# Optimization experiments

Measured on AMD Instinct MI355X. Metric: run time of the kernel, lower is better.

The kernel has to match this reference:

```python
import jax, jax.numpy as jnp
import numpy as np

B, S, D, H = 4, 2048, 1024, 16
HD = D // H


def setup_inputs() -> dict:
    key = jax.random.key(0)
    ks = jax.random.split(key, 5)
    s_in = 1.0 / np.sqrt(D)
    return {
        "x": jax.random.normal(ks[0], (B, S, D), dtype=jnp.float32),
        "W_attn": jax.random.uniform(ks[1], (D, 3 * D), dtype=jnp.float32, minval=-s_in, maxval=s_in),
        "b_attn": jax.random.uniform(ks[2], (3 * D,), dtype=jnp.float32, minval=-s_in, maxval=s_in),
        "W_proj": jax.random.uniform(ks[3], (D, D), dtype=jnp.float32, minval=-s_in, maxval=s_in),
        "b_proj": jax.random.uniform(ks[4], (D,), dtype=jnp.float32, minval=-s_in, maxval=s_in),
    }


def reference(x, W_attn, b_attn, W_proj, b_proj):
    b, s, d = x.shape
    qkv = x @ W_attn + b_attn                      # [B,S,3D]
    q, k, v = jnp.split(qkv, 3, axis=-1)
    # [B,H,S,HD]
    q = q.reshape(b, s, H, HD).transpose(0, 2, 1, 3)
    k = k.reshape(b, s, H, HD).transpose(0, 2, 1, 3)
    v = v.reshape(b, s, H, HD).transpose(0, 2, 1, 3)
    scale = 1.0 / np.sqrt(HD)
    att = jnp.einsum("bhqd,bhkd->bhqk", q, k) * scale
    causal = jnp.tril(jnp.ones((s, s), dtype=bool))
    att = jnp.where(causal[None, None], att, -jnp.inf)
    att = jax.nn.softmax(att, axis=-1)
    y = jnp.einsum("bhqk,bhkd->bhqd", att, v)      # [B,H,S,HD]
    y = y.transpose(0, 2, 1, 3).reshape(b, s, d)
    return y @ W_proj + b_proj
```

## Files before the change

kernel.cpp:

```cpp
#include <hip/hip_runtime.h>

#define B_  4
#define S_  2048
#define D_  1024
#define H_  16
#define HD_ 64
#define BS_ (B_*S_)

typedef _Float16 f16;
typedef _Float16 f16_8 __attribute__((ext_vector_type(8)));
typedef _Float16 f16_4 __attribute__((ext_vector_type(4)));
typedef float    f32_4 __attribute__((ext_vector_type(4)));
typedef unsigned int u32;

#define MFMA32(a,b,c) __builtin_amdgcn_mfma_f32_16x16x32_f16(a, b, c, 0, 0, 0)
#define MFMA16(a,b,c) __builtin_amdgcn_mfma_f32_16x16x16f16(a, b, c, 0, 0, 0)
#define NEG_INF (-__builtin_inff())

__device__ inline void gl_lds16(const f16* g, f16* lds_base, int chunk_base) {
    __builtin_amdgcn_global_load_lds(
        (const __attribute__((address_space(1))) u32*)g,
        (__attribute__((address_space(3))) u32*)(lds_base + (size_t)chunk_base * 8),
        16, 0, 0);
}

__global__ __launch_bounds__(256) void prep(
    const float* __restrict__ X,  f16* __restrict__ Xh,
    const float* __restrict__ Wa, f16* __restrict__ Wta)
{
    __shared__ f16 T[64][72];
    const int t = threadIdx.x;
    const int bid = blockIdx.x;
    if (bid < 4096) {
        const size_t i = ((size_t)bid * 256 + t) * 8;
        float4 a = *(const float4*)&X[i];
        float4 b = *(const float4*)&X[i + 4];
        f16 h[8] = {(f16)a.x,(f16)a.y,(f16)a.z,(f16)a.w,
                    (f16)b.x,(f16)b.y,(f16)b.z,(f16)b.w};
        *(uint4*)&Xh[i] = *(const uint4*)h;
        return;
    }
    const int idx = bid - 4096;
    const int n0 = (idx % 48) * 64, k0 = (idx / 48) * 64;
    const int nl4 = (t & 15) * 4;
    #pragma unroll
    for (int r = 0; r < 4; r++) {
        const int kl = (t >> 4) + r * 16;
        float4 v = *(const float4*)&Wa[(size_t)(k0 + kl) * 3072 + n0 + nl4];
        T[nl4 + 0][kl] = (f16)v.x;
        T[nl4 + 1][kl] = (f16)v.y;
        T[nl4 + 2][kl] = (f16)v.z;
        T[nl4 + 3][kl] = (f16)v.w;
    }
    __syncthreads();
    const int nr = t >> 2, kc = (t & 3) * 16;
    *(uint4*)&Wta[(size_t)(n0 + nr) * 1024 + k0 + kc]     = *(uint4*)&T[nr][kc];
    *(uint4*)&Wta[(size_t)(n0 + nr) * 1024 + k0 + kc + 8] = *(uint4*)&T[nr][kc + 8];
}

__global__ __launch_bounds__(256) void trans_w(
    const float* __restrict__ W, f16* __restrict__ Wt, int ncols)
{
    __shared__ f16 T[64][72];
    const int t = threadIdx.x;
    const int n0 = blockIdx.x * 64, k0 = blockIdx.y * 64;
    const int nl4 = (t & 15) * 4;
    #pragma unroll
    for (int r = 0; r < 4; r++) {
        const int kl = (t >> 4) + r * 16;
        float4 v = *(const float4*)&W[(size_t)(k0 + kl) * ncols + n0 + nl4];
        T[nl4 + 0][kl] = (f16)v.x;
        T[nl4 + 1][kl] = (f16)v.y;
        T[nl4 + 2][kl] = (f16)v.z;
        T[nl4 + 3][kl] = (f16)v.w;
    }
    __syncthreads();
    const int nr = t >> 2, kc = (t & 3) * 16;
    *(uint4*)&Wt[(size_t)(n0 + nr) * 1024 + k0 + kc]     = *(uint4*)&T[nr][kc];
    *(uint4*)&Wt[(size_t)(n0 + nr) * 1024 + k0 + kc + 8] = *(uint4*)&T[nr][kc + 8];
}

__global__ __launch_bounds__(512, 2) void qkv_gemm(
    const f16*   __restrict__ Xh,
    const f16*   __restrict__ Wta,
    const float* __restrict__ bias,
    f16* __restrict__ Qb, f16* __restrict__ Kb, f16* __restrict__ Vt)
{
    __shared__ f16 lds[73728];

    const int t    = threadIdx.x;
    const int lane = t & 63;
    const int w    = t >> 6;
    const int quad = lane >> 4, l15 = lane & 15;
    const int wr = w >> 2, wc = w & 3;
    const int m0 = blockIdx.x * 128;
    const int n0 = blockIdx.y * 256;
    const int wb = t & 448;

    int aoff[2], boff[4];
    #pragma unroll
    for (int c = 0; c < 2; c++) {
        const int i = c*512 + t, row = i >> 3, sl = i & 7;
        aoff[c] = row*1024 + ((sl ^ (row & 7)) << 3);
    }
    #pragma unroll
    for (int c = 0; c < 4; c++) {
        const int i = c*512 + t, row = i >> 3, sl = i & 7;
        boff[c] = row*1024 + ((sl ^ (row & 7)) << 3);
    }
    int fa[4][2], fb[4][2];
    #pragma unroll
    for (int mi = 0; mi < 4; mi++)
        #pragma unroll
        for (int kk = 0; kk < 2; kk++)
            fa[mi][kk] = (wr*64 + mi*16 + l15)*64 + (((kk*4 + quad) ^ (l15 & 7)) << 3);
    #pragma unroll
    for (int ni = 0; ni < 4; ni++)
        #pragma unroll
        for (int kk = 0; kk < 2; kk++)
            fb[ni][kk] = (wc*64 + ni*16 + l15)*64 + (((kk*4 + quad) ^ (l15 & 7)) << 3);

    const f16* Ag = Xh  + (size_t)m0 * 1024;
    const f16* Bg = Wta + (size_t)n0 * 1024;

    f32_4 acc[4][4] = {};

    #pragma unroll
    for (int c = 0; c < 2; c++) gl_lds16(Ag + aoff[c],       lds,                c*512 + wb);
    #pragma unroll
    for (int c = 0; c < 4; c++) gl_lds16(Bg + boff[c],       lds + 8192,         c*512 + wb);
    #pragma unroll
    for (int c = 0; c < 2; c++) gl_lds16(Ag + 64 + aoff[c],  lds + 24576,        c*512 + wb);
    #pragma unroll
    for (int c = 0; c < 4; c++) gl_lds16(Bg + 64 + boff[c],  lds + 24576 + 8192, c*512 + wb);
    asm volatile("s_waitcnt vmcnt(6)" ::: "memory");
    __builtin_amdgcn_s_barrier();
    asm volatile("" ::: "memory");

    int cur = 0;
    #pragma unroll 1
    for (int T = 0; T < 16; T++) {
        f16* buf        = lds + cur*24576;
        const int nxt   = cur ? cur - 1 : 2;
        f16* nbuf       = lds + nxt*24576;
        const bool st   = (T < 14);
        const int  kt2  = (T + 2) * 64;

        if (st) {
            #pragma unroll
            for (int c = 0; c < 2; c++)
                gl_lds16(Ag + kt2 + aoff[c], nbuf, c*512 + wb);
        }
        f16_8 af[4][2], bf[2][2];
        #pragma unroll
        for (int mi = 0; mi < 4; mi++)
            #pragma unroll
            for (int kk = 0; kk < 2; kk++)
                af[mi][kk] = *(const f16_8*)&buf[fa[mi][kk]];
        #pragma unroll
        for (int ni = 0; ni < 2; ni++)
            #pragma unroll
            for (int kk = 0; kk < 2; kk++)
                bf[ni][kk] = *(const f16_8*)&buf[8192 + fb[ni][kk]];
        asm volatile("" ::: "memory");
        __builtin_amdgcn_s_barrier();
        asm volatile("" ::: "memory");
        __builtin_amdgcn_s_setprio(1);
        #pragma unroll
        for (int kk = 0; kk < 2; kk++)
            #pragma unroll
            for (int mi = 0; mi < 4; mi++)
                #pragma unroll
                for (int ni = 0; ni < 2; ni++)
                    acc[mi][ni] = MFMA32(af[mi][kk], bf[ni][kk], acc[mi][ni]);
        __builtin_amdgcn_s_setprio(0);
        asm volatile("" ::: "memory");
        __builtin_amdgcn_s_barrier();
        asm volatile("" ::: "memory");

        if (st) {
            #pragma unroll
            for (int c = 0; c < 4; c++)
                gl_lds16(Bg + kt2 + boff[c], nbuf + 8192, c*512 + wb);
        }
        #pragma unroll
        for (int ni = 0; ni < 2; ni++)
            #pragma unroll
            for (int kk = 0; kk < 2; kk++)
                bf[ni][kk] = *(const f16_8*)&buf[8192 + fb[2 + ni][kk]];
        asm volatile("" ::: "memory");
        __builtin_amdgcn_s_barrier();
        asm volatile("" ::: "memory");
        __builtin_amdgcn_s_setprio(1);
        #pragma unroll
        for (int kk = 0; kk < 2; kk++)
            #pragma unroll
            for (int mi = 0; mi < 4; mi++)
                #pragma unroll
                for (int ni = 0; ni < 2; ni++)
                    acc[mi][2 + ni] = MFMA32(af[mi][kk], bf[ni][kk], acc[mi][2 + ni]);
        __builtin_amdgcn_s_setprio(0);
        if (T < 14)       asm volatile("s_waitcnt vmcnt(6)" ::: "memory");
        else if (T == 14) asm volatile("s_waitcnt vmcnt(0)" ::: "memory");
        __builtin_amdgcn_s_barrier();
        asm volatile("" ::: "memory");

        cur = (cur >= 2) ? 0 : cur + 1;
    }

    const int which = n0 >> 10;
    float bcol[4];
    #pragma unroll
    for (int ni = 0; ni < 4; ni++)
        bcol[ni] = bias[n0 + wc*64 + ni*16 + l15];

    if (which < 2) {
        f16* dstB = (which == 0) ? Qb : Kb;
        const float sc = (which == 0) ? 0.125f * 1.44269504f : 1.0f;
        f16* Ct2 = lds;
        #pragma unroll
        for (int mi = 0; mi < 4; mi++)
        #pragma unroll
        for (int ni = 0; ni < 4; ni++)
        #pragma unroll
        for (int r = 0; r < 4; r++) {
            int ml = wr*64 + mi*16 + quad*4 + r;
            int nl = wc*64 + ni*16 + l15;
            Ct2[ml*264 + nl] = (f16)((acc[mi][ni][r] + bcol[ni]) * sc);
        }
        __syncthreads();
        const int b  = m0 >> 11, s0 = m0 & 2047;
        const int h0 = (n0 & 1023) >> 6;
        #pragma unroll
        for (int c = 0; c < 8; c++) {
            const int i   = c*512 + t;
            const int row = i >> 5, j = (i >> 3) & 3, k = i & 7;
            f16* dst = dstB + ((size_t)(b*16 + h0 + j)*2048 + s0 + row)*64 + k*8;
            *(uint4*)dst = *(const uint4*)&Ct2[row*264 + j*64 + k*8];
        }
    } else {
        f16* Ct = lds;
        #pragma unroll
        for (int mi = 0; mi < 4; mi++)
        #pragma unroll
        for (int ni = 0; ni < 4; ni++)
        #pragma unroll
        for (int r = 0; r < 4; r++) {
            int nl = wc*64 + ni*16 + l15;
            int ml = wr*64 + mi*16 + quad*4 + r;
            Ct[nl*136 + ml] = (f16)(acc[mi][ni][r] + bcol[ni]);
        }
        __syncthreads();
        const int row = t >> 1, half = t & 1;
        const int nv = (n0 & 1023) + row;
        const int h = nv >> 6, hd = nv & 63;
        const int b = m0 >> 11;
        const int s0 = (m0 & 2047) + half*64;
        f16* dst = Vt + ((size_t)(b*16 + h)*64 + hd)*2048 + s0;
        #pragma unroll
        for (int j = 0; j < 8; j++)
            *(uint4*)&dst[j*8] = *(uint4*)&Ct[row*136 + half*64 + j*8];
    }
}

__global__ __launch_bounds__(256, 4) void attn(
    const f16* __restrict__ Qb,
    const f16* __restrict__ Kb,
    const f16* __restrict__ Vt,
    f16* __restrict__ Y)
{
    __shared__ f16 lds[16384];

    const int t    = threadIdx.x;
    const int w    = t >> 6;
    const int lane = t & 63;
    const int quad = lane >> 4, l15 = lane & 15;
    const int bh   = blockIdx.x;
    const int b    = bh >> 4, h = bh & 15;
    const int strip = 15 - (int)blockIdx.y;
    const int qw   = strip*128 + w*32;
    const int NT   = 2*strip + 2;

    const f16* qh = Qb + (size_t)bh * S_ * 64;
    const f16* kh = Kb + (size_t)bh * S_ * 64;
    const f16* vt = Vt + (size_t)bh * 64 * S_;

    int srcK[2], srcV[2];
    #pragma unroll
    for (int c = 0; c < 2; c++) {
        const int i = c*256 + t, row = i >> 3, sl = i & 7;
        const int sw = ((sl ^ (row & 7)) << 3);
        srcK[c] = row*64   + sw;
        srcV[c] = row*2048 + sw;
    }
    const int wbase = t & 192;
    const int l7    = l15 & 7;
    const f16_4 ones = {(f16)1,(f16)1,(f16)1,(f16)1};

    f16_8 qa[2][2];
    #pragma unroll
    for (int rt = 0; rt < 2; rt++)
        #pragma unroll
        for (int c = 0; c < 2; c++)
            qa[rt][c] = *(const f16_8*)&qh[(size_t)(qw + rt*16 + l15)*64 + c*32 + quad*8];

    f32_4 o[2][4] = {};
    f32_4 lacc[2] = {};

    #pragma unroll
    for (int c = 0; c < 2; c++) {
        gl_lds16(kh + srcK[c], lds,        c*256 + wbase);
        gl_lds16(vt + srcV[c], lds + 4096, c*256 + wbase);
    }

    #pragma unroll 1
    for (int kt = 0; kt < NT; kt++) {
        const int kbase = kt * 64;
        f16* Ks = lds + (kt & 1) * 8192;
        f16* Vs = Ks + 4096;

        if (kt + 1 < NT) {
            const int nb = kbase + 64;
            f16* nK = lds + ((kt + 1) & 1) * 8192;
            #pragma unroll
            for (int c = 0; c < 2; c++) {
                gl_lds16(kh + (size_t)nb*64 + srcK[c], nK,        c*256 + wbase);
                gl_lds16(vt + nb + srcV[c],            nK + 4096, c*256 + wbase);
            }
            asm volatile("s_waitcnt vmcnt(4)" ::: "memory");
        } else {
            asm volatile("s_waitcnt vmcnt(0)" ::: "memory");
        }
        __builtin_amdgcn_s_barrier();
        asm volatile("" ::: "memory");

        if (kbase <= qw + 31) {
            f16_8 kb[4][2];
            #pragma unroll
            for (int sub = 0; sub < 4; sub++)
                #pragma unroll
                for (int c = 0; c < 2; c++)
                    kb[sub][c] = *(const f16_8*)
                        &Ks[(sub*16 + l15)*64 + (((c*4 + quad) ^ l7) << 3)];
            f32_4 st[2][4];
            __builtin_amdgcn_s_setprio(1);
            #pragma unroll
            for (int rt = 0; rt < 2; rt++)
                #pragma unroll
                for (int sub = 0; sub < 4; sub++) {
                    f32_4 a = {};
                    a = MFMA32(kb[sub][0], qa[rt][0], a);
                    a = MFMA32(kb[sub][1], qa[rt][1], a);
                    st[rt][sub] = a;
                }
            __builtin_amdgcn_s_setprio(0);

            const bool masked = (kbase + 63 > qw);
            f16_4 pt[2][4];
            #pragma unroll
            for (int rt = 0; rt < 2; rt++)
            #pragma unroll
            for (int sub = 0; sub < 4; sub++) {
                const int qrow = qw + rt*16 + l15;
                f16_4 p;
                #pragma unroll
                for (int r = 0; r < 4; r++) {
                    float x = st[rt][sub][r];
                    if (masked) {
                        int key = kbase + sub*16 + quad*4 + r;
                        x = (key <= qrow) ? x : NEG_INF;
                    }
                    p[r] = (f16)__builtin_amdgcn_exp2f(x);
                }
                pt[rt][sub] = p;
            }

            #pragma unroll
            for (int rt = 0; rt < 2; rt++) {
                f16_4 ps = (pt[rt][0] + pt[rt][1]) + (pt[rt][2] + pt[rt][3]);
                lacc[rt] = MFMA16(ps, ones, lacc[rt]);
            }

            __builtin_amdgcn_s_setprio(1);
            #pragma unroll
            for (int sub = 0; sub < 4; sub++) {
                f16_4 vb[4];
                #pragma unroll
                for (int tt = 0; tt < 4; tt++)
                    vb[tt] = *(const f16_4*)
                        &Vs[(tt*16 + l15)*64 +
                            ((((sub*2 + (quad >> 1)) ^ l7) << 3) + (quad & 1)*4)];
                #pragma unroll
                for (int rt = 0; rt < 2; rt++)
                    #pragma unroll
                    for (int tt = 0; tt < 4; tt++)
                        o[rt][tt] = MFMA16(pt[rt][sub], vb[tt], o[rt][tt]);
            }
            __builtin_amdgcn_s_setprio(0);
        }
        asm volatile("" ::: "memory");
        __builtin_amdgcn_s_barrier();
        asm volatile("" ::: "memory");
    }

    #pragma unroll
    for (int rt = 0; rt < 2; rt++)
    #pragma unroll
    for (int r = 0; r < 4; r++) {
        float inv = 1.0f / lacc[rt][r];
        int srw = qw + rt*16 + quad*4 + r;
        #pragma unroll
        for (int tt = 0; tt < 4; tt++)
            Y[(size_t)(b*S_ + srw)*1024 + h*64 + tt*16 + l15] =
                (f16)(o[rt][tt][r] * inv);
    }
}

__global__ __launch_bounds__(512, 2) void proj_gemm(
    const f16* __restrict__ Yb,
    const f16* __restrict__ Wtp,
    const float* __restrict__ bias,
    float* __restrict__ Out)
{
    __shared__ f16 lds[73728];

    const int t    = threadIdx.x;
    const int lane = t & 63;
    const int w    = t >> 6;
    const int quad = lane >> 4, l15 = lane & 15;
    const int wr = w >> 2, wc = w & 3;
    const int m0 = blockIdx.x * 128;
    const int n0 = blockIdx.y * 256;
    const int wb = t & 448;

    int aoff[2], boff[4];
    #pragma unroll
    for (int c = 0; c < 2; c++) {
        const int i = c*512 + t, row = i >> 3, sl = i & 7;
        aoff[c] = row*1024 + ((sl ^ (row & 7)) << 3);
    }
    #pragma unroll
    for (int c = 0; c < 4; c++) {
        const int i = c*512 + t, row = i >> 3, sl = i & 7;
        boff[c] = row*1024 + ((sl ^ (row & 7)) << 3);
    }
    int fa[4][2], fb[4][2];
    #pragma unroll
    for (int mi = 0; mi < 4; mi++)
        #pragma unroll
        for (int kk = 0; kk < 2; kk++)
            fa[mi][kk] = (wr*64 + mi*16 + l15)*64 + (((kk*4 + quad) ^ (l15 & 7)) << 3);
    #pragma unroll
    for (int ni = 0; ni < 4; ni++)
        #pragma unroll
        for (int kk = 0; kk < 2; kk++)
            fb[ni][kk] = (wc*64 + ni*16 + l15)*64 + (((kk*4 + quad) ^ (l15 & 7)) << 3);

    const f16* Ag = Yb  + (size_t)m0 * 1024;
    const f16* Bg = Wtp + (size_t)n0 * 1024;

    f32_4 acc[4][4] = {};

    #pragma unroll
    for (int c = 0; c < 2; c++) gl_lds16(Ag + aoff[c],       lds,                c*512 + wb);
    #pragma unroll
    for (int c = 0; c < 4; c++) gl_lds16(Bg + boff[c],       lds + 8192,         c*512 + wb);
    #pragma unroll
    for (int c = 0; c < 2; c++) gl_lds16(Ag + 64 + aoff[c],  lds + 24576,        c*512 + wb);
    #pragma unroll
    for (int c = 0; c < 4; c++) gl_lds16(Bg + 64 + boff[c],  lds + 24576 + 8192, c*512 + wb);
    asm volatile("s_waitcnt vmcnt(6)" ::: "memory");
    __builtin_amdgcn_s_barrier();
    asm volatile("" ::: "memory");

    int cur = 0;
    #pragma unroll 1
    for (int T = 0; T < 16; T++) {
        f16* buf        = lds + cur*24576;
        const int nxt   = cur ? cur - 1 : 2;
        f16* nbuf       = lds + nxt*24576;
        const bool st   = (T < 14);
        const int  kt2  = (T + 2) * 64;

        if (st) {
            #pragma unroll
            for (int c = 0; c < 2; c++)
                gl_lds16(Ag + kt2 + aoff[c], nbuf, c*512 + wb);
        }
        f16_8 af[4][2], bf[2][2];
        #pragma unroll
        for (int mi = 0; mi < 4; mi++)
            #pragma unroll
            for (int kk = 0; kk < 2; kk++)
                af[mi][kk] = *(const f16_8*)&buf[fa[mi][kk]];
        #pragma unroll
        for (int ni = 0; ni < 2; ni++)
            #pragma unroll
            for (int kk = 0; kk < 2; kk++)
                bf[ni][kk] = *(const f16_8*)&buf[8192 + fb[ni][kk]];
        asm volatile("" ::: "memory");
        __builtin_amdgcn_s_barrier();
        asm volatile("" ::: "memory");
        __builtin_amdgcn_s_setprio(1);
        #pragma unroll
        for (int kk = 0; kk < 2; kk++)
            #pragma unroll
            for (int mi = 0; mi < 4; mi++)
                #pragma unroll
                for (int ni = 0; ni < 2; ni++)
                    acc[mi][ni] = MFMA32(af[mi][kk], bf[ni][kk], acc[mi][ni]);
        __builtin_amdgcn_s_setprio(0);
        asm volatile("" ::: "memory");
        __builtin_amdgcn_s_barrier();
        asm volatile("" ::: "memory");

        if (st) {
            #pragma unroll
            for (int c = 0; c < 4; c++)
                gl_lds16(Bg + kt2 + boff[c], nbuf + 8192, c*512 + wb);
        }
        #pragma unroll
        for (int ni = 0; ni < 2; ni++)
            #pragma unroll
            for (int kk = 0; kk < 2; kk++)
                bf[ni][kk] = *(const f16_8*)&buf[8192 + fb[2 + ni][kk]];
        asm volatile("" ::: "memory");
        __builtin_amdgcn_s_barrier();
        asm volatile("" ::: "memory");
        __builtin_amdgcn_s_setprio(1);
        #pragma unroll
        for (int kk = 0; kk < 2; kk++)
            #pragma unroll
            for (int mi = 0; mi < 4; mi++)
                #pragma unroll
                for (int ni = 0; ni < 2; ni++)
                    acc[mi][2 + ni] = MFMA32(af[mi][kk], bf[ni][kk], acc[mi][2 + ni]);
        __builtin_amdgcn_s_setprio(0);
        if (T < 14)       asm volatile("s_waitcnt vmcnt(6)" ::: "memory");
        else if (T == 14) asm volatile("s_waitcnt vmcnt(0)" ::: "memory");
        __builtin_amdgcn_s_barrier();
        asm volatile("" ::: "memory");

        cur = (cur >= 2) ? 0 : cur + 1;
    }

    #pragma unroll
    for (int mi = 0; mi < 4; mi++)
    #pragma unroll
    for (int ni = 0; ni < 4; ni++)
    #pragma unroll
    for (int r = 0; r < 4; r++) {
        int m = m0 + wr*64 + mi*16 + quad*4 + r;
        int n = n0 + wc*64 + ni*16 + l15;
        Out[(size_t)m*1024 + n] = acc[mi][ni][r] + bias[n];
    }
}

extern "C" void kernel_launch(void* const* d_in, const int* in_sizes, int n_in,
                              void* d_out, int out_size, void* d_ws, size_t ws_size,
                              hipStream_t stream) {
    const float* x      = (const float*)d_in[0];
    const float* W_attn = (const float*)d_in[1];
    const float* b_attn = (const float*)d_in[2];
    const float* W_proj = (const float*)d_in[3];
    const float* b_proj = (const float*)d_in[4];
    float* out = (float*)d_out;

    const size_t per = (size_t)B_ * H_ * S_ * HD_;
    f16* Yb  = (f16*)d_ws;
    f16* Wta = Yb;
    f16* Qb  = Yb + per;
    f16* Kb  = Qb + per;
    f16* Vt  = Kb + per;
    f16* Wtp = Qb;
    f16* Xh  = (f16*)d_out;

    prep     <<<4096 + 768, 256, 0, stream>>>(x, Xh, W_attn, Wta);
    qkv_gemm <<<dim3(64, 12), 512, 0, stream>>>(Xh, Wta, b_attn, Qb, Kb, Vt);
    attn     <<<dim3(64, 16), 256, 0, stream>>>(Qb, Kb, Vt, Yb);
    trans_w  <<<dim3(16, 16), 256, 0, stream>>>(W_proj, Wtp, D_);
    proj_gemm<<<dim3(64, 4),  512, 0, stream>>>(Yb, Wtp, b_proj, out);
}
```

Measured before the change: 254.7 us.

## Triple-buffer K/V tiles in attention and fold W_proj transpose into prep

The attention kernel moves from double to triple buffering of K/V tiles in LDS, prefetching two tiles ahead with adjusted vmcnt waits, to hide global load latency. LDS per block grows from 32KB to 48KB, which may cut occupancy below the 4-blocks-per-CU launch bound. Separately, when the workspace is large enough, the W_proj transpose/convert runs inside the prep kernel instead of a separate launch, removing one kernel launch.

```diff
diff --git a/kernel.cpp b/kernel.cpp
--- a/kernel.cpp
+++ b/kernel.cpp
@@ -26,7 +26,8 @@
 
 __global__ __launch_bounds__(256) void prep(
     const float* __restrict__ X,  f16* __restrict__ Xh,
-    const float* __restrict__ Wa, f16* __restrict__ Wta)
+    const float* __restrict__ Wa, f16* __restrict__ Wta,
+    const float* __restrict__ Wp, f16* __restrict__ Wtp)
 {
     __shared__ f16 T[64][72];
     const int t = threadIdx.x;
@@ -40,13 +41,23 @@
         *(uint4*)&Xh[i] = *(const uint4*)h;
         return;
     }
-    const int idx = bid - 4096;
-    const int n0 = (idx % 48) * 64, k0 = (idx / 48) * 64;
+    int n0, k0, ncols;
+    const float* Wsrc;
+    f16* Wdst;
+    if (bid < 4864) {
+        const int idx = bid - 4096;
+        n0 = (idx % 48) * 64; k0 = (idx / 48) * 64;
+        ncols = 3072; Wsrc = Wa; Wdst = Wta;
+    } else {
+        const int idx = bid - 4864;
+        n0 = (idx % 16) * 64; k0 = (idx / 16) * 64;
+        ncols = 1024; Wsrc = Wp; Wdst = Wtp;
+    }
     const int nl4 = (t & 15) * 4;
     #pragma unroll
     for (int r = 0; r < 4; r++) {
         const int kl = (t >> 4) + r * 16;
-        float4 v = *(const float4*)&Wa[(size_t)(k0 + kl) * 3072 + n0 + nl4];
+        float4 v = *(const float4*)&Wsrc[(size_t)(k0 + kl) * ncols + n0 + nl4];
         T[nl4 + 0][kl] = (f16)v.x;
         T[nl4 + 1][kl] = (f16)v.y;
         T[nl4 + 2][kl] = (f16)v.z;
@@ -54,8 +65,8 @@
     }
     __syncthreads();
     const int nr = t >> 2, kc = (t & 3) * 16;
-    *(uint4*)&Wta[(size_t)(n0 + nr) * 1024 + k0 + kc]     = *(uint4*)&T[nr][kc];
-    *(uint4*)&Wta[(size_t)(n0 + nr) * 1024 + k0 + kc + 8] = *(uint4*)&T[nr][kc + 8];
+    *(uint4*)&Wdst[(size_t)(n0 + nr) * 1024 + k0 + kc]     = *(uint4*)&T[nr][kc];
+    *(uint4*)&Wdst[(size_t)(n0 + nr) * 1024 + k0 + kc + 8] = *(uint4*)&T[nr][kc + 8];
 }
 
 __global__ __launch_bounds__(256) void trans_w(
@@ -269,7 +280,7 @@
     const f16* __restrict__ Vt,
     f16* __restrict__ Y)
 {
-    __shared__ f16 lds[16384];
+    __shared__ f16 lds[24576];
 
     const int t    = threadIdx.x;
     const int w    = t >> 6;
@@ -312,21 +323,28 @@
         gl_lds16(kh + srcK[c], lds,        c*256 + wbase);
         gl_lds16(vt + srcV[c], lds + 4096, c*256 + wbase);
     }
+    #pragma unroll
+    for (int c = 0; c < 2; c++) {
+        gl_lds16(kh + 64*64 + srcK[c], lds + 8192,        c*256 + wbase);
+        gl_lds16(vt + 64    + srcV[c], lds + 8192 + 4096, c*256 + wbase);
+    }
 
     #pragma unroll 1
     for (int kt = 0; kt < NT; kt++) {
         const int kbase = kt * 64;
-        f16* Ks = lds + (kt & 1) * 8192;
+        f16* Ks = lds + (kt % 3) * 8192;
         f16* Vs = Ks + 4096;
 
-        if (kt + 1 < NT) {
-            const int nb = kbase + 64;
-            f16* nK = lds + ((kt + 1) & 1) * 8192;
+        if (kt + 2 < NT) {
+            const int nb = kbase + 128;
+            f16* nK = lds + ((kt + 2) % 3) * 8192;
             #pragma unroll
             for (int c = 0; c < 2; c++) {
                 gl_lds16(kh + (size_t)nb*64 + srcK[c], nK,        c*256 + wbase);
                 gl_lds16(vt + nb + srcV[c],            nK + 4096, c*256 + wbase);
             }
+            asm volatile("s_waitcnt vmcnt(8)" ::: "memory");
+        } else if (kt + 1 < NT) {
             asm volatile("s_waitcnt vmcnt(4)" ::: "memory");
         } else {
             asm volatile("s_waitcnt vmcnt(0)" ::: "memory");
@@ -572,12 +590,16 @@
     f16* Qb  = Yb + per;
     f16* Kb  = Qb + per;
     f16* Vt  = Kb + per;
-    f16* Wtp = Qb;
     f16* Xh  = (f16*)d_out;
 
-    prep     <<<4096 + 768, 256, 0, stream>>>(x, Xh, W_attn, Wta);
+    const bool big = ws_size >= (4*per + (size_t)D_*D_) * sizeof(f16);
+    f16* Wtp = big ? (Vt + per) : Qb;
+
+    prep     <<<4096 + 768 + (big ? 256 : 0), 256, 0, stream>>>(
+                 x, Xh, W_attn, Wta, W_proj, Wtp);
     qkv_gemm <<<dim3(64, 12), 512, 0, stream>>>(Xh, Wta, b_attn, Qb, Kb, Vt);
     attn     <<<dim3(64, 16), 256, 0, stream>>>(Qb, Kb, Vt, Yb);
-    trans_w  <<<dim3(16, 16), 256, 0, stream>>>(W_proj, Wtp, D_);
+    if (!big)
+        trans_w<<<dim3(16, 16), 256, 0, stream>>>(W_proj, Wtp, D_);
     proj_gemm<<<dim3(64, 4),  512, 0, stream>>>(Yb, Wtp, b_proj, out);
 }
```

Measured after the change: 260.8 us. 2.4% more time.
